# Performance work log

Hardware: AMD Instinct MI355X
Metric: run time of the kernel (lower is better)

The kernel has to match this reference:

```python
import jax, jax.numpy as jnp
import numpy as np

B, S, D, H = 8, 1024, 2048, 16
DH = D // H  # 128


def setup_inputs() -> dict:
    key = jax.random.key(0)
    ks = jax.random.split(key, 6)
    sc = 1.0 / np.sqrt(D)
    return {
        "q": jax.random.normal(ks[0], (B, S, D), jnp.float32),
        "k": jax.random.normal(ks[1], (B, S, D), jnp.float32),
        "v": jax.random.normal(ks[2], (B, S, D), jnp.float32),
        "Wq": jax.random.normal(ks[3], (D, D), jnp.float32) * sc,
        "Wk": jax.random.normal(ks[4], (D, D), jnp.float32) * sc,
        "Wv": jax.random.normal(ks[5], (D, D), jnp.float32) * sc,
    }


def reference(q, k, v, Wq, Wk, Wv):
    # Linear projections (no bias), then split feature dim into H heads of DH.
    qh = (q @ Wq).reshape(B, S, H, DH)
    kh = (k @ Wk).reshape(B, S, H, DH)
    vh = (v @ Wv).reshape(B, S, H, DH)
    # scores: [B, H, Sq, Sk], scaled by sqrt(d_head)
    scores = jnp.einsum("bqhd,bkhd->bhqk", qh, kh) / jnp.sqrt(
        jnp.asarray(DH, qh.dtype)
    )
    probs = jax.nn.softmax(scores, axis=-1)
    out = jnp.einsum("bhqk,bkhd->bqhd", probs, vh).reshape(B, S, D)
    return out.astype(jnp.float32)
```

## Files before the change

### kernel.cpp

```cpp
#include <hip/hip_runtime.h>
#include <hip/hip_bf16.h>
#include <math.h>

#define BB 8
#define SS 1024
#define DD 2048
#define HH 16
#define DHD 128

typedef float  v4f  __attribute__((ext_vector_type(4)));
typedef short  v4s  __attribute__((ext_vector_type(4)));
typedef short  v8s  __attribute__((ext_vector_type(8)));
typedef __bf16 v8bf __attribute__((ext_vector_type(8)));

#define GLOBAL_AS __attribute__((address_space(1)))
#define LDS_AS    __attribute__((address_space(3)))

__device__ __forceinline__ unsigned short f2b(float f) {
    union { float f; unsigned int u; } x; x.f = f;
    unsigned int r = x.u + 0x7fffu + ((x.u >> 16) & 1u);
    return (unsigned short)(r >> 16);
}

__device__ __forceinline__ v8bf ldsv8(const unsigned short* p) {
    return __builtin_bit_cast(v8bf, *(const v8s*)p);
}

__global__ __launch_bounds__(256) void cvt_f32_bf16(const float* __restrict__ src,
                                                    unsigned short* __restrict__ dst,
                                                    int n4) {
    int i = blockIdx.x * blockDim.x + threadIdx.x;
    int stride = gridDim.x * blockDim.x;
    for (; i < n4; i += stride) {
        v4f f = ((const v4f*)src)[i];
        v4s o;
        o[0] = (short)f2b(f[0]); o[1] = (short)f2b(f[1]);
        o[2] = (short)f2b(f[2]); o[3] = (short)f2b(f[3]);
        ((v4s*)dst)[i] = o;
    }
}

__global__ __launch_bounds__(256) void wtrans_kernel(const float* __restrict__ W,
                                                     unsigned short* __restrict__ WT) {
    __shared__ float t[64][65];
    int nb = blockIdx.x * 64;
    int kb = blockIdx.y * 64;
    int tr = threadIdx.x >> 4;
    int tc = (threadIdx.x & 15) * 4;
#pragma unroll
    for (int i = 0; i < 4; i++) {
        int k = kb + tr + i * 16;
        v4f v = *(const v4f*)(W + (size_t)k * DD + nb + tc);
        t[tr + i * 16][tc + 0] = v[0];
        t[tr + i * 16][tc + 1] = v[1];
        t[tr + i * 16][tc + 2] = v[2];
        t[tr + i * 16][tc + 3] = v[3];
    }
    __syncthreads();
#pragma unroll
    for (int i = 0; i < 4; i++) {
        int n = nb + tr + i * 16;
        v4s o;
#pragma unroll
        for (int j = 0; j < 4; j++) o[j] = (short)f2b(t[tc + j][tr + i * 16]);
        *(v4s*)(WT + (size_t)n * DD + kb + tc) = o;
    }
}


#define STAGE_A(bb, gg, tt) do {                                              \
    __builtin_amdgcn_global_load_lds(                                         \
        (const GLOBAL_AS void*)(pA0 + (size_t)(gg) * 64 * K + (size_t)(tt) * 64), \
        (LDS_AS void*)(&sA[(bb) * 16384 + ldsA0 + (gg) * 4096]), 16, 0, 0);   \
    __builtin_amdgcn_global_load_lds(                                         \
        (const GLOBAL_AS void*)(pA1 + (size_t)(gg) * 64 * K + (size_t)(tt) * 64), \
        (LDS_AS void*)(&sA[(bb) * 16384 + ldsA1 + (gg) * 4096]), 16, 0, 0);   \
} while (0)

#define STAGE_B(bb, gg, tt) do {                                              \
    __builtin_amdgcn_global_load_lds(                                         \
        (const GLOBAL_AS void*)(pB0 + (size_t)(gg) * 32 * K + (size_t)(tt) * 64), \
        (LDS_AS void*)(&sB[(bb) * 16384 + ldsB0 + (gg) * 2048]), 16, 0, 0);   \
    __builtin_amdgcn_global_load_lds(                                         \
        (const GLOBAL_AS void*)(pB1 + (size_t)(gg) * 32 * K + (size_t)(tt) * 64), \
        (LDS_AS void*)(&sB[(bb) * 16384 + ldsB1 + (gg) * 2048]), 16, 0, 0);   \
} while (0)

#define PHASE(mh, nh, dolda, STAGE_STMT, TAIL_STMT) do {                      \
    if (dolda) {                                                              \
        _Pragma("unroll")                                                     \
        for (int i = 0; i < 4; i++) {                                         \
            af[i][0] = ldsv8(sAb + aRow + (mh) * 4096 + i * 1024 + c0);       \
            af[i][1] = ldsv8(sAb + aRow + (mh) * 4096 + i * 1024 + c1);       \
        }                                                                     \
    }                                                                         \
    _Pragma("unroll")                                                         \
    for (int j = 0; j < 2; j++) {                                             \
        bf2[j][0] = ldsv8(sBb + bRow + (nh) * 2048 + j * 1024 + c0);          \
        bf2[j][1] = ldsv8(sBb + bRow + (nh) * 2048 + j * 1024 + c1);          \
    }                                                                         \
    STAGE_STMT;                                                               \
    __builtin_amdgcn_s_barrier();                                             \
    asm volatile("s_waitcnt lgkmcnt(0)");                                     \
    __builtin_amdgcn_sched_barrier(0);                                        \
    __builtin_amdgcn_s_setprio(1);                                            \
    _Pragma("unroll")                                                         \
    for (int i = 0; i < 4; i++) {                                             \
        _Pragma("unroll")                                                     \
        for (int j = 0; j < 2; j++) {                                         \
            acc[(mh) * 4 + i][(nh) * 2 + j] =                                 \
                __builtin_amdgcn_mfma_f32_16x16x32_bf16(                      \
                    af[i][0], bf2[j][0], acc[(mh) * 4 + i][(nh) * 2 + j], 0, 0, 0); \
            acc[(mh) * 4 + i][(nh) * 2 + j] =                                 \
                __builtin_amdgcn_mfma_f32_16x16x32_bf16(                      \
                    af[i][1], bf2[j][1], acc[(mh) * 4 + i][(nh) * 2 + j], 0, 0, 0); \
        }                                                                     \
    }                                                                         \
    __builtin_amdgcn_s_setprio(0);                                            \
    TAIL_STMT;                                                                \
    __builtin_amdgcn_s_barrier();                                             \
} while (0)

__global__ __launch_bounds__(512, 2) void gemm256(const unsigned short* __restrict__ A,
                                                  const unsigned short* __restrict__ BT,
                                                  unsigned short* __restrict__ C,
                                                  float scale, int vmode,
                                                  int M, int N, int K) {
    __shared__ __align__(16) unsigned short sA[2 * 16384];
    __shared__ __align__(16) unsigned short sB[2 * 16384];

    const int tid  = threadIdx.x;
    const int lane = tid & 63;
    const int w    = tid >> 6;
    const int qcol = lane & 15;
    const int quad = lane >> 4;
    const int l3   = lane >> 3;
    const int l7   = lane & 7;

    const int ntn = N >> 8;
    const int bn  = (blockIdx.x % ntn) * 256;
    const int bm  = (blockIdx.x / ntn) * 256;

    const int wm = (w >> 2) * 128;
    const int wn = (w & 3) * 64;

    const int gchunk = (l7 ^ l3) * 8;
    const int iA0 = w * 2, iA1 = w * 2 + 1;
    const int raA0 = (iA0 >> 3) * 128 + (iA0 & 7) * 8;
    const int raA1 = (iA1 >> 3) * 128 + (iA1 & 7) * 8;
    const int rbB0 = (iA0 >> 2) * 64 + (iA0 & 3) * 8;
    const int rbB1 = (iA1 >> 2) * 64 + (iA1 & 3) * 8;
    const unsigned short* pA0 = A  + (size_t)(bm + raA0 + l3) * K + gchunk;
    const unsigned short* pA1 = A  + (size_t)(bm + raA1 + l3) * K + gchunk;
    const unsigned short* pB0 = BT + (size_t)(bn + rbB0 + l3) * K + gchunk;
    const unsigned short* pB1 = BT + (size_t)(bn + rbB1 + l3) * K + gchunk;
    const int ldsA0 = raA0 * 64, ldsA1 = raA1 * 64;
    const int ldsB0 = rbB0 * 64, ldsB1 = rbB1 * 64;

    const int c0   = ((quad ^ l7) & 7) * 8;
    const int c1   = c0 ^ 32;
    const int aRow = (wm + qcol) * 64;
    const int bRow = (wn + qcol) * 64;

    v4f acc[8][4];
#pragma unroll
    for (int i = 0; i < 8; i++)
#pragma unroll
        for (int j = 0; j < 4; j++) acc[i][j] = (v4f){0.f, 0.f, 0.f, 0.f};

    v8bf af[4][2];
    v8bf bf2[2][2];

    const int nt = K >> 6;

    STAGE_A(0, 0, 0); STAGE_B(0, 0, 0);
    STAGE_A(0, 1, 0); STAGE_B(0, 1, 0);
    STAGE_A(1, 0, 1); STAGE_B(1, 0, 1);
    asm volatile("s_waitcnt vmcnt(4)");
    __builtin_amdgcn_sched_barrier(0);
    __builtin_amdgcn_s_barrier();

    for (int t = 0; t < nt; ++t) {
        const int buf = t & 1, nbuf = buf ^ 1;
        const unsigned short* sAb = &sA[buf * 16384];
        const unsigned short* sBb = &sB[buf * 16384];
        const bool st1 = (t + 1 < nt);
        const bool st2 = (t + 2 < nt);

        PHASE(0, 0, 1, if (st1) STAGE_A(nbuf, 1, t + 1), );
        PHASE(0, 1, 0, if (st1) STAGE_B(nbuf, 1, t + 1), );
        PHASE(1, 0, 1, if (st2) STAGE_A(buf, 0, t + 2), );
        PHASE(1, 1, 0, if (st2) STAGE_B(buf, 0, t + 2),
              if (t < nt - 2) { asm volatile("s_waitcnt vmcnt(4)"); }
              else            { asm volatile("s_waitcnt vmcnt(0)"); }
              __builtin_amdgcn_sched_barrier(0));
    }

    if (vmode == 0) {
#pragma unroll
        for (int mi = 0; mi < 8; mi++)
#pragma unroll
            for (int nj = 0; nj < 4; nj++)
#pragma unroll
                for (int r = 0; r < 4; r++) {
                    int row = bm + wm + mi * 16 + quad * 4 + r;
                    int col = bn + wn + nj * 16 + qcol;
                    C[(size_t)row * N + col] = f2b(acc[mi][nj][r] * scale);
                }
    } else {
#pragma unroll
        for (int mi = 0; mi < 8; mi++)
#pragma unroll
            for (int nj = 0; nj < 4; nj++)
#pragma unroll
                for (int r = 0; r < 4; r++) {
                    int row = bm + wm + mi * 16 + quad * 4 + r;
                    int col = bn + wn + nj * 16 + qcol;
                    size_t idx = ((size_t)(row >> 10) * 2048 + col) * 1024 + (row & 1023);
                    C[idx] = f2b(acc[mi][nj][r] * scale);
                }
    }
}

__global__ __launch_bounds__(256, 4) void attn_kernel(const unsigned short* __restrict__ qh,
                                                      const unsigned short* __restrict__ kh,
                                                      const unsigned short* __restrict__ vt,
                                                      float* __restrict__ out) {
    __shared__ __align__(16) unsigned short sK[64 * 128];
    __shared__ __align__(16) unsigned short sV[128 * 64];

    int lane = threadIdx.x & 63, w = threadIdx.x >> 6;
    int b = blockIdx.z, h = blockIdx.y;
    int q0 = blockIdx.x * 64 + w * 16;
    int qcol = lane & 15, quad = lane >> 4;

    const unsigned short* qp = qh + (size_t)(b * SS + q0 + qcol) * DD + h * DHD;
    v8bf bq[4];
#pragma unroll
    for (int kk = 0; kk < 4; kk++)
        bq[kk] = __builtin_bit_cast(v8bf, *(const v8s*)(qp + kk * 32 + quad * 8));

    int ko[4];
#pragma unroll
    for (int j = 0; j < 4; j++) {
        int key = w * 16 + j * 4 + (lane >> 4);
        ko[j] = key * DD + (((lane & 15) ^ (key & 15)) * 8);
    }
    int vo0 = (w * 32 + (lane >> 3)) * SS + (((lane & 7) ^ (lane >> 3)) * 8);

    const unsigned short* kcur = kh + (size_t)b * SS * DD + h * DHD;
    const unsigned short* vcur = vt + (size_t)(b * HH + h) * DHD * SS;
    unsigned short* kl0 = &sK[(w * 16) * 128];
    unsigned short* vl0 = &sV[(w * 32) * 64];

    float m_i = -1e30f, l_i = 0.f;
    v4f acc[8];
#pragma unroll
    for (int c = 0; c < 8; c++) acc[c] = (v4f){0.f, 0.f, 0.f, 0.f};

    for (int kb = 0; kb < SS; kb += 64) {
        __syncthreads();
#pragma unroll
        for (int j = 0; j < 4; j++)
            __builtin_amdgcn_global_load_lds((const GLOBAL_AS void*)(kcur + ko[j]),
                                             (LDS_AS void*)(kl0 + j * 4 * 128), 16, 0, 0);
#pragma unroll
        for (int j = 0; j < 4; j++)
            __builtin_amdgcn_global_load_lds((const GLOBAL_AS void*)(vcur + vo0 + j * 8 * SS),
                                             (LDS_AS void*)(vl0 + j * 8 * 64), 16, 0, 0);
        kcur += (size_t)64 * DD;
        vcur += 64;
        __syncthreads();

        v4f s[4];
#pragma unroll
        for (int kf = 0; kf < 4; kf++) {
            s[kf] = (v4f){0.f, 0.f, 0.f, 0.f};
#pragma unroll
            for (int kk = 0; kk < 4; kk++) {
                v8bf ak = __builtin_bit_cast(v8bf,
                    *(const v8s*)&sK[(kf * 16 + qcol) * 128 + (((kk * 4 + quad) ^ qcol) * 8)]);
                s[kf] = __builtin_amdgcn_mfma_f32_16x16x32_bf16(ak, bq[kk], s[kf], 0, 0, 0);
            }
        }

        float mx = -1e30f;
#pragma unroll
        for (int kf = 0; kf < 4; kf++)
#pragma unroll
            for (int r = 0; r < 4; r++) mx = fmaxf(mx, s[kf][r]);
        mx = fmaxf(mx, __shfl_xor(mx, 16));
        mx = fmaxf(mx, __shfl_xor(mx, 32));
        float m_new = fmaxf(m_i, mx);
        float rs = 0.f;
        v4s p[4];
#pragma unroll
        for (int kf = 0; kf < 4; kf++)
#pragma unroll
            for (int r = 0; r < 4; r++) {
                float pf = exp2f(s[kf][r] - m_new);
                rs += pf;
                p[kf][r] = (short)f2b(pf);
            }
        rs += __shfl_xor(rs, 16);
        rs += __shfl_xor(rs, 32);
        float alpha = exp2f(m_i - m_new);
        l_i = l_i * alpha + rs;
        m_i = m_new;
#pragma unroll
        for (int c = 0; c < 8; c++) {
            acc[c][0] *= alpha; acc[c][1] *= alpha;
            acc[c][2] *= alpha; acc[c][3] *= alpha;
        }

#pragma unroll
        for (int c = 0; c < 8; c++) {
            int row = (c * 16 + qcol) * 64;
#pragma unroll
            for (int kf = 0; kf < 4; kf++) {
                v4s av = *(const v4s*)&sV[row + (((kf * 2 + (quad >> 1)) ^ (qcol & 7)) * 8)
                                              + (quad & 1) * 4];
                acc[c] = __builtin_amdgcn_mfma_f32_16x16x16bf16_1k(av, p[kf], acc[c], 0, 0, 0);
            }
        }
    }

    float rl = 1.0f / l_i;
    float* op = out + (size_t)(b * SS + q0 + qcol) * DD + h * DHD;
#pragma unroll
    for (int c = 0; c < 8; c++)
#pragma unroll
        for (int r = 0; r < 4; r++)
            op[c * 16 + quad * 4 + r] = acc[c][r] * rl;
}

extern "C" void kernel_launch(void* const* d_in, const int* in_sizes, int n_in,
                              void* d_out, int out_size, void* d_ws, size_t ws_size,
                              hipStream_t stream) {
    const float* ins[3]  = {(const float*)d_in[0], (const float*)d_in[1], (const float*)d_in[2]};
    const float* wins[3] = {(const float*)d_in[3], (const float*)d_in[4], (const float*)d_in[5]};
    char* ws = (char*)d_ws;
    unsigned short* abuf = (unsigned short*)(ws);
    unsigned short* wbuf = (unsigned short*)(ws + (size_t)32 * 1024 * 1024);
    unsigned short* qhb  = (unsigned short*)(ws + (size_t)40 * 1024 * 1024);
    unsigned short* khb  = (unsigned short*)(ws + (size_t)72 * 1024 * 1024);
    unsigned short* vtb  = (unsigned short*)(ws + (size_t)104 * 1024 * 1024);
    float* out = (float*)d_out;

    unsigned short* outs[3] = {qhb, khb, vtb};
    const float qscale = 0.12753139626246937f;
    float scales[3] = {qscale, 1.f, 1.f};
    int   vmodes[3] = {0, 0, 1};

    const int M = BB * SS, N = DD, K = DD;
    const int grid = (M / 256) * (N / 256);

    for (int i = 0; i < 3; i++) {
        cvt_f32_bf16<<<dim3(4096), dim3(256), 0, stream>>>(ins[i], abuf, (BB * SS * DD) / 4);
        wtrans_kernel<<<dim3(32, 32), dim3(256), 0, stream>>>(wins[i], wbuf);
        gemm256<<<dim3(grid), dim3(512), 0, stream>>>(abuf, wbuf, outs[i],
                                                      scales[i], vmodes[i], M, N, K);
    }
    attn_kernel<<<dim3(SS / 64, HH, BB), dim3(256), 0, stream>>>(qhb, khb, vtb, out);
}
```

Before: 637.7 us.

## Restructure GEMM pipeline: stage-first phases, reuse fragments, grouped tile order

Each phase of the GEMM main loop now issues its global-to-LDS staging first. It drops the per-phase lgkmcnt wait and the extra barrier, and changes the phase order (00, 01, 11, 10) so the A or B fragments already in registers are reused across adjacent phases. Prefetch now targets only the next buffer, and the final k-tile runs as a separate epilogue with its own vmcnt waits. The MFMA loops are split into two passes over the K halves. Block indices are remapped so consecutive blocks share B column tiles, which should improve L2 reuse. The waitcnt bookkeeping is fragile: relying on implicit LDS waits and a single barrier per phase risks ordering hazards.

```diff
diff --git a/kernel.cpp b/kernel.cpp
--- a/kernel.cpp
+++ b/kernel.cpp
@@ -86,38 +86,41 @@
         (LDS_AS void*)(&sB[(bb) * 16384 + ldsB1 + (gg) * 2048]), 16, 0, 0);   \
 } while (0)
 
-#define PHASE(mh, nh, dolda, STAGE_STMT, TAIL_STMT) do {                      \
-    if (dolda) {                                                              \
+#define PHASE(mh, nh, DOLDA, DOLDB, STAGE_STMT, WAIT_STMT) do {               \
+    STAGE_STMT;                                                               \
+    if (DOLDA) {                                                              \
         _Pragma("unroll")                                                     \
         for (int i = 0; i < 4; i++) {                                         \
             af[i][0] = ldsv8(sAb + aRow + (mh) * 4096 + i * 1024 + c0);       \
             af[i][1] = ldsv8(sAb + aRow + (mh) * 4096 + i * 1024 + c1);       \
         }                                                                     \
     }                                                                         \
-    _Pragma("unroll")                                                         \
-    for (int j = 0; j < 2; j++) {                                             \
-        bf2[j][0] = ldsv8(sBb + bRow + (nh) * 2048 + j * 1024 + c0);          \
-        bf2[j][1] = ldsv8(sBb + bRow + (nh) * 2048 + j * 1024 + c1);          \
+    if (DOLDB) {                                                              \
+        _Pragma("unroll")                                                     \
+        for (int j = 0; j < 2; j++) {                                         \
+            bf2[j][0] = ldsv8(sBb + bRow + (nh) * 2048 + j * 1024 + c0);      \
+            bf2[j][1] = ldsv8(sBb + bRow + (nh) * 2048 + j * 1024 + c1);      \
+        }                                                                     \
     }                                                                         \
-    STAGE_STMT;                                                               \
-    __builtin_amdgcn_s_barrier();                                             \
-    asm volatile("s_waitcnt lgkmcnt(0)");                                     \
-    __builtin_amdgcn_sched_barrier(0);                                        \
     __builtin_amdgcn_s_setprio(1);                                            \
     _Pragma("unroll")                                                         \
     for (int i = 0; i < 4; i++) {                                             \
         _Pragma("unroll")                                                     \
-        for (int j = 0; j < 2; j++) {                                         \
+        for (int j = 0; j < 2; j++)                                           \
             acc[(mh) * 4 + i][(nh) * 2 + j] =                                 \
                 __builtin_amdgcn_mfma_f32_16x16x32_bf16(                      \
                     af[i][0], bf2[j][0], acc[(mh) * 4 + i][(nh) * 2 + j], 0, 0, 0); \
+    }                                                                         \
+    _Pragma("unroll")                                                         \
+    for (int i = 0; i < 4; i++) {                                             \
+        _Pragma("unroll")                                                     \
+        for (int j = 0; j < 2; j++)                                           \
             acc[(mh) * 4 + i][(nh) * 2 + j] =                                 \
                 __builtin_amdgcn_mfma_f32_16x16x32_bf16(                      \
                     af[i][1], bf2[j][1], acc[(mh) * 4 + i][(nh) * 2 + j], 0, 0, 0); \
-        }                                                                     \
     }                                                                         \
     __builtin_amdgcn_s_setprio(0);                                            \
-    TAIL_STMT;                                                                \
+    WAIT_STMT;                                                                \
     __builtin_amdgcn_s_barrier();                                             \
 } while (0)
 
@@ -137,9 +140,9 @@
     const int l3   = lane >> 3;
     const int l7   = lane & 7;
 
-    const int ntn = N >> 8;
-    const int bn  = (blockIdx.x % ntn) * 256;
-    const int bm  = (blockIdx.x / ntn) * 256;
+    const int bid = blockIdx.x;
+    const int bm  = ((bid & 7) * 4 + ((bid >> 3) & 3)) * 256;
+    const int bn  = (bid >> 5) * 256;
 
     const int wm = (w >> 2) * 128;
     const int wn = (w & 3) * 64;
@@ -173,27 +176,35 @@
 
     const int nt = K >> 6;
 
-    STAGE_A(0, 0, 0); STAGE_B(0, 0, 0);
-    STAGE_A(0, 1, 0); STAGE_B(0, 1, 0);
-    STAGE_A(1, 0, 1); STAGE_B(1, 0, 1);
+    STAGE_A(0, 0, 0);
+    STAGE_B(0, 0, 0);
+    STAGE_B(0, 1, 0);
+    STAGE_A(0, 1, 0);
     asm volatile("s_waitcnt vmcnt(4)");
-    __builtin_amdgcn_sched_barrier(0);
     __builtin_amdgcn_s_barrier();
 
-    for (int t = 0; t < nt; ++t) {
+    for (int t = 0; t < nt - 1; ++t) {
         const int buf = t & 1, nbuf = buf ^ 1;
         const unsigned short* sAb = &sA[buf * 16384];
         const unsigned short* sBb = &sB[buf * 16384];
-        const bool st1 = (t + 1 < nt);
-        const bool st2 = (t + 2 < nt);
-
-        PHASE(0, 0, 1, if (st1) STAGE_A(nbuf, 1, t + 1), );
-        PHASE(0, 1, 0, if (st1) STAGE_B(nbuf, 1, t + 1), );
-        PHASE(1, 0, 1, if (st2) STAGE_A(buf, 0, t + 2), );
-        PHASE(1, 1, 0, if (st2) STAGE_B(buf, 0, t + 2),
-              if (t < nt - 2) { asm volatile("s_waitcnt vmcnt(4)"); }
-              else            { asm volatile("s_waitcnt vmcnt(0)"); }
-              __builtin_amdgcn_sched_barrier(0));
+
+        PHASE(0, 0, 1, 1, STAGE_A(nbuf, 0, t + 1),
+              asm volatile("s_waitcnt vmcnt(4)"));
+        PHASE(0, 1, 0, 1, STAGE_B(nbuf, 0, t + 1),
+              asm volatile("s_waitcnt vmcnt(4)"));
+        PHASE(1, 1, 1, 0, STAGE_B(nbuf, 1, t + 1), );
+        PHASE(1, 0, 0, 1, STAGE_A(nbuf, 1, t + 1),
+              asm volatile("s_waitcnt vmcnt(4)"));
+    }
+
+    {
+        const int buf = (nt - 1) & 1;
+        const unsigned short* sAb = &sA[buf * 16384];
+        const unsigned short* sBb = &sB[buf * 16384];
+        PHASE(0, 0, 1, 1, , asm volatile("s_waitcnt vmcnt(2)"));
+        PHASE(0, 1, 0, 1, , asm volatile("s_waitcnt vmcnt(0)"));
+        PHASE(1, 1, 1, 0, , );
+        PHASE(1, 0, 0, 1, , );
     }
 
     if (vmode == 0) {
```

Result: faster. 624.0 us (-2.2%).
